# Kernel optimization log

Measured on AMD Instinct MI355X. Metric: run time of the kernel, lower is better.

## Reference

```python
import jax, jax.numpy as jnp
import numpy as np
import math

NUM_HEADS = 16


def _alibi_slopes(n):
    # n is a power of 2 here (16)
    start = 2.0 ** (-2.0 ** (-(math.log2(n) - 3)))
    return jnp.asarray([start * (start ** i) for i in range(n)], dtype=jnp.float32)


def setup_inputs() -> dict:
    key = jax.random.key(0)
    ks = jax.random.split(key, 7)
    B, S, D = 2, 2048, 1024
    s = 0.02
    return {
        "query": jax.random.normal(ks[0], (B, S, D), jnp.float32),
        "key": jax.random.normal(ks[1], (B, S, D), jnp.float32),
        "value": jax.random.normal(ks[2], (B, S, D), jnp.float32),
        "Wq": jax.random.normal(ks[3], (D, D), jnp.float32) * s,
        "Wk": jax.random.normal(ks[4], (D, D), jnp.float32) * s,
        "Wv": jax.random.normal(ks[5], (D, D), jnp.float32) * s,
        "Wo": jax.random.normal(ks[6], (D, D), jnp.float32) * s,
    }


def reference(query, key, value, Wq, Wk, Wv, Wo):
    B, S, D = query.shape
    H = NUM_HEADS
    hd = D // H
    scale = math.sqrt(hd)

    # projections (bias-free linears), split into heads: [B, S, H, hd]
    Q = (query @ Wq).reshape(B, S, H, hd)
    K = (key @ Wk).reshape(B, -1, H, hd)
    V = (value @ Wv).reshape(B, -1, H, hd)

    # attention scores [B, H, S, S]
    scores = jnp.einsum("bqhd,bkhd->bhqk", Q, K) / scale

    # ALiBi bias: -slope_h * |i - j|, broadcast over batch
    pos = jnp.arange(S, dtype=jnp.float32)
    rel = jnp.abs(pos[None, :] - pos[:, None])  # [S, S]
    slopes = _alibi_slopes(H)
    scores = scores - slopes[None, :, None, None] * rel[None, None, :, :]

    attn = jax.nn.softmax(scores, axis=-1)
    out = jnp.einsum("bhqk,bkhd->bqhd", attn, V).reshape(B, S, D)
    return out @ Wo
```

## Files before the change

### kernel.cpp

```cpp
#include <hip/hip_runtime.h>
#include <cstdint>
#include <cstddef>


typedef unsigned short u16;
typedef __attribute__((ext_vector_type(8))) _Float16 half8;
typedef __attribute__((ext_vector_type(4))) float f32x4;

#define DEVI static __device__ __forceinline__
#define MFMA16(a, b, c) __builtin_amdgcn_mfma_f32_16x16x32_f16(a, b, c, 0, 0, 0)

DEVI u16 f2h_bits(float f) {
  _Float16 h = (_Float16)f;
  union { _Float16 h; u16 u; } v; v.h = h;
  return v.u;
}

DEVI void gl_lds16(const u16* g, u16* l) {
  __builtin_amdgcn_global_load_lds(
      (const __attribute__((address_space(1))) void*)g,
      (__attribute__((address_space(3))) void*)l, 16, 0, 0);
}

__global__ __launch_bounds__(256) void cast3_h(const float* __restrict__ in0,
                                               const float* __restrict__ in1,
                                               const float* __restrict__ in2,
                                               u16* __restrict__ o0,
                                               u16* __restrict__ o1,
                                               u16* __restrict__ o2, int n) {
  const float* in = blockIdx.z == 0 ? in0 : (blockIdx.z == 1 ? in1 : in2);
  u16* out = blockIdx.z == 0 ? o0 : (blockIdx.z == 1 ? o1 : o2);
  int i = (blockIdx.x * 256 + threadIdx.x) * 4;
  if (i + 3 < n) {
    const float4 v = *(const float4*)(in + i);
    ushort4 o;
    o.x = f2h_bits(v.x); o.y = f2h_bits(v.y); o.z = f2h_bits(v.z); o.w = f2h_bits(v.w);
    *(ushort4*)(out + i) = o;
  }
}

__global__ __launch_bounds__(256) void transpose4_h(
    const float* __restrict__ W0, const float* __restrict__ W1,
    const float* __restrict__ W2, const float* __restrict__ W3,
    u16* __restrict__ T0, u16* __restrict__ T1, u16* __restrict__ T2,
    u16* __restrict__ T3) {
  const float* W = blockIdx.z == 0 ? W0 : (blockIdx.z == 1 ? W1 : (blockIdx.z == 2 ? W2 : W3));
  u16* Wt = blockIdx.z == 0 ? T0 : (blockIdx.z == 1 ? T1 : (blockIdx.z == 2 ? T2 : T3));
  __shared__ float tile[32][33];
  const int bx = blockIdx.x * 32;
  const int by = blockIdx.y * 32;
  const int x = threadIdx.x & 31;
  const int y0 = threadIdx.x >> 5;
#pragma unroll
  for (int i = y0; i < 32; i += 8)
    tile[i][x] = W[(size_t)(by + i) * 1024 + bx + x];
  __syncthreads();
#pragma unroll
  for (int i = y0; i < 32; i += 8)
    Wt[(size_t)(bx + i) * 1024 + by + x] = f2h_bits(tile[x][i]);
}

DEVI void gemm_body(const u16* __restrict__ A, const u16* __restrict__ Bt,
                    void* __restrict__ Cout, int mode, u16* As, u16* Bs) {
  constexpr int K = 1024, N = 1024;
  const int t = threadIdx.x;
  const int lane = t & 63;
  const int quad = lane >> 4;
  const int l16 = lane & 15;
  const int wid = t >> 6;
  const int mBase = blockIdx.y * 128;
  const int nBase = blockIdx.x * 128;
  const int wM = (wid >> 1) * 64;
  const int wN = (wid & 1) * 64;
  const int aswz = (quad ^ ((l16 >> 1) & 3)) << 3;

  f32x4 acc[4][4];
#pragma unroll
  for (int i = 0; i < 4; ++i)
#pragma unroll
    for (int j = 0; j < 4; ++j) acc[i][j] = (f32x4){0.f, 0.f, 0.f, 0.f};

  for (int kt = 0; kt < K / 32; ++kt) {
    const int kB = kt * 32;
    __syncthreads();
#pragma unroll
    for (int i = 0; i < 2; ++i) {
      const int ci = i * 256 + t;
      const int row = ci >> 2;
      const int col = (((ci & 3) ^ ((ci >> 3) & 3)) << 3);
      gl_lds16(A + (size_t)(mBase + row) * K + kB + col, As + ci * 8);
      gl_lds16(Bt + (size_t)(nBase + row) * K + kB + col, Bs + ci * 8);
    }
    __syncthreads();

    half8 a[4], b[4];
#pragma unroll
    for (int mi = 0; mi < 4; ++mi)
      a[mi] = *(const half8*)(As + (wM + mi * 16 + l16) * 32 + aswz);
#pragma unroll
    for (int ni = 0; ni < 4; ++ni)
      b[ni] = *(const half8*)(Bs + (wN + ni * 16 + l16) * 32 + aswz);
#pragma unroll
    for (int mi = 0; mi < 4; ++mi)
#pragma unroll
      for (int ni = 0; ni < 4; ++ni)
        acc[mi][ni] = MFMA16(a[mi], b[ni], acc[mi][ni]);
  }

#pragma unroll
  for (int mi = 0; mi < 4; ++mi) {
#pragma unroll
    for (int ni = 0; ni < 4; ++ni) {
#pragma unroll
      for (int r = 0; r < 4; ++r) {
        const int m = mBase + wM + mi * 16 + quad * 4 + r;
        const int n = nBase + wN + ni * 16 + l16;
        const float v = acc[mi][ni][r];
        if (mode == 0) {
          ((float*)Cout)[(size_t)m * N + n] = v;
        } else if (mode == 1) {
          ((u16*)Cout)[(size_t)m * N + n] = f2h_bits(v);
        } else {
          ((u16*)Cout)[(((size_t)(m >> 11) * 1024 + n) << 11) | (size_t)(m & 2047)] = f2h_bits(v);
        }
      }
    }
  }
}

__global__ __launch_bounds__(256) void proj_qkv(
    const u16* __restrict__ qb, const u16* __restrict__ kb, const u16* __restrict__ vb,
    const u16* __restrict__ Wqt, const u16* __restrict__ Wkt, const u16* __restrict__ Wvt,
    u16* __restrict__ Qp, u16* __restrict__ Kp, u16* __restrict__ Vtp) {
  __shared__ u16 As[128 * 32];
  __shared__ u16 Bs[128 * 32];
  const int z = blockIdx.z;
  const u16* A = z == 0 ? qb : (z == 1 ? kb : vb);
  const u16* Bt = z == 0 ? Wqt : (z == 1 ? Wkt : Wvt);
  void* C = z == 0 ? (void*)Qp : (z == 1 ? (void*)Kp : (void*)Vtp);
  gemm_body(A, Bt, C, z == 2 ? 2 : 1, As, Bs);
}

__global__ __launch_bounds__(256) void gemm_out(const u16* __restrict__ Ao,
                                                const u16* __restrict__ Wot,
                                                float* __restrict__ out) {
  __shared__ u16 As[128 * 32];
  __shared__ u16 Bs[128 * 32];
  gemm_body(Ao, Wot, out, 0, As, Bs);
}

__global__ __launch_bounds__(128, 2) void flash_alibi(
    const u16* __restrict__ Qg, const u16* __restrict__ Kg,
    const u16* __restrict__ Vtg, u16* __restrict__ Og) {
  constexpr int S = 2048, Dm = 1024, HD = 64;
  __shared__ u16 Qs[64 * 64];
  __shared__ u16 Ks[64 * 64];
  __shared__ u16 Vs[64 * 64];
  __shared__ u16 Ps[64 * 64];
  const int t = threadIdx.x, lane = t & 63, wid = t >> 6;
  const int quad = lane >> 4, l16 = lane & 15;
  const int qt = blockIdx.x, h = blockIdx.y, b = blockIdx.z;
  const int qBase = qt * 64;
  const size_t qRow0 = (size_t)b * S + qBase;
  const float sl2 = __builtin_amdgcn_exp2f(-0.5f * (float)(h + 1)) * 1.44269504f;
  const float sc2 = 0.125f * 1.44269504f;
  const int Di = (int)(30.0f / sl2);
  const int ktLo = max(0, (qBase - Di) >> 6);
  const int ktHi = min(31, (qBase + 63 + Di) >> 6);
  const int cswz = ((l16 & 7) << 3);

#pragma unroll
  for (int i = 0; i < 4; ++i) {
    const int ci = i * 128 + t;
    const int row = ci >> 3, col = (((ci & 7) ^ (row & 7)) << 3);
    gl_lds16(Qg + (qRow0 + row) * Dm + h * HD + col, Qs + ci * 8);
  }

  float bi[2][4];
#pragma unroll
  for (int m = 0; m < 2; ++m)
#pragma unroll
    for (int r = 0; r < 4; ++r)
      bi[m][r] = sl2 * (float)(qBase + wid * 32 + m * 16 + quad * 4 + r);

  f32x4 acc_o[2][4];
#pragma unroll
  for (int m = 0; m < 2; ++m)
#pragma unroll
    for (int nd = 0; nd < 4; ++nd) acc_o[m][nd] = (f32x4){0.f, 0.f, 0.f, 0.f};
  float lrow[2][4] = {{0.f, 0.f, 0.f, 0.f}, {0.f, 0.f, 0.f, 0.f}};

  const int pRowBase = wid * 32;

  for (int kt = ktLo; kt <= ktHi; ++kt) {
    const int kB = kt * 64;
    __syncthreads();
#pragma unroll
    for (int i = 0; i < 4; ++i) {
      const int ci = i * 128 + t;
      const int row = ci >> 3, col = (((ci & 7) ^ (row & 7)) << 3);
      gl_lds16(Kg + ((size_t)b * S + kB + row) * Dm + h * HD + col, Ks + ci * 8);
      gl_lds16(Vtg + ((size_t)(b * 16 + h) * HD + row) * S + kB + col, Vs + ci * 8);
    }
    __syncthreads();

    f32x4 s[2][4];
#pragma unroll
    for (int m = 0; m < 2; ++m)
#pragma unroll
      for (int ni = 0; ni < 4; ++ni) s[m][ni] = (f32x4){0.f, 0.f, 0.f, 0.f};
#pragma unroll
    for (int ks = 0; ks < 2; ++ks) {
      const int ck = ((ks * 4 + quad) << 3) ^ cswz;
      const half8 a0 = *(const half8*)(Qs + (wid * 32 + l16) * HD + ck);
      const half8 a1 = *(const half8*)(Qs + (wid * 32 + 16 + l16) * HD + ck);
#pragma unroll
      for (int ni = 0; ni < 4; ++ni) {
        const half8 bk = *(const half8*)(Ks + (ni * 16 + l16) * HD + ck);
        s[0][ni] = MFMA16(a0, bk, s[0][ni]);
        s[1][ni] = MFMA16(a1, bk, s[1][ni]);
      }
    }

    float bj[4];
#pragma unroll
    for (int ni = 0; ni < 4; ++ni) bj[ni] = sl2 * (float)(kB + ni * 16 + l16);
#pragma unroll
    for (int m = 0; m < 2; ++m) {
#pragma unroll
      for (int r = 0; r < 4; ++r) {
        float rs = 0.f;
        const int prow = (pRowBase + m * 16 + quad * 4 + r) * 64;
#pragma unroll
        for (int ni = 0; ni < 4; ++ni) {
          const float d = fabsf(bi[m][r] - bj[ni]);
          const float p = __builtin_amdgcn_exp2f(s[m][ni][r] * sc2 - d);
          rs += p;
          Ps[prow + ((ni * 16 + l16) ^ (quad << 4))] = f2h_bits(p);
        }
        lrow[m][r] += rs;
      }
    }
    __asm__ volatile("s_waitcnt lgkmcnt(0)" ::: "memory");

#pragma unroll
    for (int ks = 0; ks < 2; ++ks) {
      const int pk = (ks * 32 + quad * 8) ^ ((l16 & 12) << 2);
      const int ck = ((ks * 4 + quad) << 3) ^ cswz;
      const half8 aP0 = *(const half8*)(Ps + (pRowBase + l16) * 64 + pk);
      const half8 aP1 = *(const half8*)(Ps + (pRowBase + 16 + l16) * 64 + pk);
#pragma unroll
      for (int nd = 0; nd < 4; ++nd) {
        const half8 bv = *(const half8*)(Vs + (nd * 16 + l16) * HD + ck);
        acc_o[0][nd] = MFMA16(aP0, bv, acc_o[0][nd]);
        acc_o[1][nd] = MFMA16(aP1, bv, acc_o[1][nd]);
      }
    }
  }

#pragma unroll
  for (int m = 0; m < 2; ++m) {
#pragma unroll
    for (int r = 0; r < 4; ++r) {
      float l = lrow[m][r];
      l += __shfl_xor(l, 1);
      l += __shfl_xor(l, 2);
      l += __shfl_xor(l, 4);
      l += __shfl_xor(l, 8);
      const float inv = 1.f / l;
      const int rloc = wid * 32 + m * 16 + quad * 4 + r;
#pragma unroll
      for (int nd = 0; nd < 4; ++nd)
        Og[(qRow0 + rloc) * Dm + h * HD + nd * 16 + l16] = f2h_bits(acc_o[m][nd][r] * inv);
    }
  }
}

extern "C" void kernel_launch(void* const* d_in, const int* in_sizes, int n_in,
                              void* d_out, int out_size, void* d_ws, size_t ws_size,
                              hipStream_t stream) {
  const float* q  = (const float*)d_in[0];
  const float* k  = (const float*)d_in[1];
  const float* v  = (const float*)d_in[2];
  const float* Wq = (const float*)d_in[3];
  const float* Wk = (const float*)d_in[4];
  const float* Wv = (const float*)d_in[5];
  const float* Wo = (const float*)d_in[6];
  char* ws = (char*)d_ws;
  const size_t MB = 1ull << 20;
  u16* qb  = (u16*)(ws + 0 * MB);
  u16* kb  = (u16*)(ws + 8 * MB);
  u16* vb  = (u16*)(ws + 16 * MB);
  u16* Wqt = (u16*)(ws + 24 * MB);
  u16* Wkt = (u16*)(ws + 26 * MB);
  u16* Wvt = (u16*)(ws + 28 * MB);
  u16* Wot = (u16*)(ws + 30 * MB);
  u16* Qp  = (u16*)(ws + 32 * MB);
  u16* Kp  = (u16*)(ws + 40 * MB);
  u16* Vtp = (u16*)(ws + 48 * MB);
  u16* Ao  = (u16*)(ws + 56 * MB);

  const int n = 2 * 2048 * 1024;
  cast3_h<<<dim3(n / 1024, 1, 3), 256, 0, stream>>>(q, k, v, qb, kb, vb, n);
  transpose4_h<<<dim3(32, 32, 4), 256, 0, stream>>>(Wq, Wk, Wv, Wo, Wqt, Wkt, Wvt, Wot);
  proj_qkv<<<dim3(8, 32, 3), 256, 0, stream>>>(qb, kb, vb, Wqt, Wkt, Wvt, Qp, Kp, Vtp);
  flash_alibi<<<dim3(32, 16, 2), 128, 0, stream>>>(Qp, Kp, Vtp, Ao);
  gemm_out<<<dim3(8, 32), 256, 0, stream>>>(Ao, Wot, (float*)d_out);
}
```

Before: 244.3 us.

## Double-buffer K/V tiles in ALiBi flash kernel with four waves per block

The attention kernel now uses 256 threads with each wave handling 16 query rows instead of 32. K and V tiles are double-buffered in LDS so the next tile's global-to-LDS load is issued before computing the current one, leaving one barrier per iteration. Head order is reversed so the heads with the widest key windows are scheduled first, and s_setprio raises priority around the MFMA sections. This aims to hide load latency and improve occupancy and load balance, at the cost of more LDS and less register reuse of K/V fragments per wave.

```diff
diff --git a/kernel.cpp b/kernel.cpp
--- a/kernel.cpp
+++ b/kernel.cpp
@@ -149,17 +149,18 @@
   gemm_body(Ao, Wot, out, 0, As, Bs);
 }
 
-__global__ __launch_bounds__(128, 2) void flash_alibi(
+__global__ __launch_bounds__(256, 3) void flash_alibi(
     const u16* __restrict__ Qg, const u16* __restrict__ Kg,
     const u16* __restrict__ Vtg, u16* __restrict__ Og) {
   constexpr int S = 2048, Dm = 1024, HD = 64;
   __shared__ u16 Qs[64 * 64];
-  __shared__ u16 Ks[64 * 64];
-  __shared__ u16 Vs[64 * 64];
+  __shared__ u16 Ks[2][64 * 64];
+  __shared__ u16 Vs[2][64 * 64];
   __shared__ u16 Ps[64 * 64];
   const int t = threadIdx.x, lane = t & 63, wid = t >> 6;
   const int quad = lane >> 4, l16 = lane & 15;
-  const int qt = blockIdx.x, h = blockIdx.y, b = blockIdx.z;
+  const int qt = blockIdx.x, b = blockIdx.z;
+  const int h = 15 - blockIdx.y;
   const int qBase = qt * 64;
   const size_t qRow0 = (size_t)b * S + qBase;
   const float sl2 = __builtin_amdgcn_exp2f(-0.5f * (float)(h + 1)) * 1.44269504f;
@@ -168,111 +169,118 @@
   const int ktLo = max(0, (qBase - Di) >> 6);
   const int ktHi = min(31, (qBase + 63 + Di) >> 6);
   const int cswz = ((l16 & 7) << 3);
-
-#pragma unroll
-  for (int i = 0; i < 4; ++i) {
-    const int ci = i * 128 + t;
+  const int pRowBase = wid * 16;
+
+#pragma unroll
+  for (int i = 0; i < 2; ++i) {
+    const int ci = i * 256 + t;
     const int row = ci >> 3, col = (((ci & 7) ^ (row & 7)) << 3);
     gl_lds16(Qg + (qRow0 + row) * Dm + h * HD + col, Qs + ci * 8);
   }
-
-  float bi[2][4];
-#pragma unroll
-  for (int m = 0; m < 2; ++m)
-#pragma unroll
-    for (int r = 0; r < 4; ++r)
-      bi[m][r] = sl2 * (float)(qBase + wid * 32 + m * 16 + quad * 4 + r);
-
-  f32x4 acc_o[2][4];
-#pragma unroll
-  for (int m = 0; m < 2; ++m)
-#pragma unroll
-    for (int nd = 0; nd < 4; ++nd) acc_o[m][nd] = (f32x4){0.f, 0.f, 0.f, 0.f};
-  float lrow[2][4] = {{0.f, 0.f, 0.f, 0.f}, {0.f, 0.f, 0.f, 0.f}};
-
-  const int pRowBase = wid * 32;
+  {
+    const int kB = ktLo * 64;
+#pragma unroll
+    for (int i = 0; i < 2; ++i) {
+      const int ci = i * 256 + t;
+      const int row = ci >> 3, col = (((ci & 7) ^ (row & 7)) << 3);
+      gl_lds16(Kg + ((size_t)b * S + kB + row) * Dm + h * HD + col, Ks[0] + ci * 8);
+      gl_lds16(Vtg + ((size_t)(b * 16 + h) * HD + row) * S + kB + col, Vs[0] + ci * 8);
+    }
+  }
+
+  float bi[4];
+#pragma unroll
+  for (int r = 0; r < 4; ++r)
+    bi[r] = sl2 * (float)(qBase + wid * 16 + quad * 4 + r);
+
+  f32x4 acc_o[4];
+#pragma unroll
+  for (int nd = 0; nd < 4; ++nd) acc_o[nd] = (f32x4){0.f, 0.f, 0.f, 0.f};
+  float lrow[4] = {0.f, 0.f, 0.f, 0.f};
+
+  __syncthreads();
+  int bb = 0;
 
   for (int kt = ktLo; kt <= ktHi; ++kt) {
     const int kB = kt * 64;
-    __syncthreads();
-#pragma unroll
-    for (int i = 0; i < 4; ++i) {
-      const int ci = i * 128 + t;
-      const int row = ci >> 3, col = (((ci & 7) ^ (row & 7)) << 3);
-      gl_lds16(Kg + ((size_t)b * S + kB + row) * Dm + h * HD + col, Ks + ci * 8);
-      gl_lds16(Vtg + ((size_t)(b * 16 + h) * HD + row) * S + kB + col, Vs + ci * 8);
-    }
-    __syncthreads();
-
-    f32x4 s[2][4];
-#pragma unroll
-    for (int m = 0; m < 2; ++m)
-#pragma unroll
-      for (int ni = 0; ni < 4; ++ni) s[m][ni] = (f32x4){0.f, 0.f, 0.f, 0.f};
+    if (kt < ktHi) {
+      const int kBn = kB + 64;
+#pragma unroll
+      for (int i = 0; i < 2; ++i) {
+        const int ci = i * 256 + t;
+        const int row = ci >> 3, col = (((ci & 7) ^ (row & 7)) << 3);
+        gl_lds16(Kg + ((size_t)b * S + kBn + row) * Dm + h * HD + col, Ks[bb ^ 1] + ci * 8);
+        gl_lds16(Vtg + ((size_t)(b * 16 + h) * HD + row) * S + kBn + col, Vs[bb ^ 1] + ci * 8);
+      }
+    }
+
+    const u16* Kb = Ks[bb];
+    const u16* Vb = Vs[bb];
+
+    f32x4 s4[4];
+#pragma unroll
+    for (int ni = 0; ni < 4; ++ni) s4[ni] = (f32x4){0.f, 0.f, 0.f, 0.f};
+    __builtin_amdgcn_s_setprio(1);
 #pragma unroll
     for (int ks = 0; ks < 2; ++ks) {
       const int ck = ((ks * 4 + quad) << 3) ^ cswz;
-      const half8 a0 = *(const half8*)(Qs + (wid * 32 + l16) * HD + ck);
-      const half8 a1 = *(const half8*)(Qs + (wid * 32 + 16 + l16) * HD + ck);
+      const half8 a0 = *(const half8*)(Qs + (wid * 16 + l16) * HD + ck);
 #pragma unroll
       for (int ni = 0; ni < 4; ++ni) {
-        const half8 bk = *(const half8*)(Ks + (ni * 16 + l16) * HD + ck);
-        s[0][ni] = MFMA16(a0, bk, s[0][ni]);
-        s[1][ni] = MFMA16(a1, bk, s[1][ni]);
-      }
-    }
+        const half8 bk = *(const half8*)(Kb + (ni * 16 + l16) * HD + ck);
+        s4[ni] = MFMA16(a0, bk, s4[ni]);
+      }
+    }
+    __builtin_amdgcn_s_setprio(0);
 
     float bj[4];
 #pragma unroll
     for (int ni = 0; ni < 4; ++ni) bj[ni] = sl2 * (float)(kB + ni * 16 + l16);
 #pragma unroll
-    for (int m = 0; m < 2; ++m) {
-#pragma unroll
-      for (int r = 0; r < 4; ++r) {
-        float rs = 0.f;
-        const int prow = (pRowBase + m * 16 + quad * 4 + r) * 64;
-#pragma unroll
-        for (int ni = 0; ni < 4; ++ni) {
-          const float d = fabsf(bi[m][r] - bj[ni]);
-          const float p = __builtin_amdgcn_exp2f(s[m][ni][r] * sc2 - d);
-          rs += p;
-          Ps[prow + ((ni * 16 + l16) ^ (quad << 4))] = f2h_bits(p);
-        }
-        lrow[m][r] += rs;
-      }
+    for (int r = 0; r < 4; ++r) {
+      float rs = 0.f;
+      const int prow = (pRowBase + quad * 4 + r) * 64;
+#pragma unroll
+      for (int ni = 0; ni < 4; ++ni) {
+        const float d = fabsf(bi[r] - bj[ni]);
+        const float p = __builtin_amdgcn_exp2f(s4[ni][r] * sc2 - d);
+        rs += p;
+        Ps[prow + ((ni * 16 + l16) ^ (quad << 4))] = f2h_bits(p);
+      }
+      lrow[r] += rs;
     }
     __asm__ volatile("s_waitcnt lgkmcnt(0)" ::: "memory");
 
+    __builtin_amdgcn_s_setprio(1);
 #pragma unroll
     for (int ks = 0; ks < 2; ++ks) {
       const int pk = (ks * 32 + quad * 8) ^ ((l16 & 12) << 2);
       const int ck = ((ks * 4 + quad) << 3) ^ cswz;
-      const half8 aP0 = *(const half8*)(Ps + (pRowBase + l16) * 64 + pk);
-      const half8 aP1 = *(const half8*)(Ps + (pRowBase + 16 + l16) * 64 + pk);
+      const half8 aP = *(const half8*)(Ps + (pRowBase + l16) * 64 + pk);
 #pragma unroll
       for (int nd = 0; nd < 4; ++nd) {
-        const half8 bv = *(const half8*)(Vs + (nd * 16 + l16) * HD + ck);
-        acc_o[0][nd] = MFMA16(aP0, bv, acc_o[0][nd]);
-        acc_o[1][nd] = MFMA16(aP1, bv, acc_o[1][nd]);
-      }
-    }
-  }
-
-#pragma unroll
-  for (int m = 0; m < 2; ++m) {
-#pragma unroll
-    for (int r = 0; r < 4; ++r) {
-      float l = lrow[m][r];
-      l += __shfl_xor(l, 1);
-      l += __shfl_xor(l, 2);
-      l += __shfl_xor(l, 4);
-      l += __shfl_xor(l, 8);
-      const float inv = 1.f / l;
-      const int rloc = wid * 32 + m * 16 + quad * 4 + r;
-#pragma unroll
-      for (int nd = 0; nd < 4; ++nd)
-        Og[(qRow0 + rloc) * Dm + h * HD + nd * 16 + l16] = f2h_bits(acc_o[m][nd][r] * inv);
-    }
+        const half8 bv = *(const half8*)(Vb + (nd * 16 + l16) * HD + ck);
+        acc_o[nd] = MFMA16(aP, bv, acc_o[nd]);
+      }
+    }
+    __builtin_amdgcn_s_setprio(0);
+
+    __syncthreads();
+    bb ^= 1;
+  }
+
+#pragma unroll
+  for (int r = 0; r < 4; ++r) {
+    float l = lrow[r];
+    l += __shfl_xor(l, 1);
+    l += __shfl_xor(l, 2);
+    l += __shfl_xor(l, 4);
+    l += __shfl_xor(l, 8);
+    const float inv = 1.f / l;
+    const int rloc = wid * 16 + quad * 4 + r;
+#pragma unroll
+    for (int nd = 0; nd < 4; ++nd)
+      Og[(qRow0 + rloc) * Dm + h * HD + nd * 16 + l16] = f2h_bits(acc_o[nd][r] * inv);
   }
 }
 
@@ -304,6 +312,6 @@
   cast3_h<<<dim3(n / 1024, 1, 3), 256, 0, stream>>>(q, k, v, qb, kb, vb, n);
   transpose4_h<<<dim3(32, 32, 4), 256, 0, stream>>>(Wq, Wk, Wv, Wo, Wqt, Wkt, Wvt, Wot);
   proj_qkv<<<dim3(8, 32, 3), 256, 0, stream>>>(qb, kb, vb, Wqt, Wkt, Wvt, Qp, Kp, Vtp);
-  flash_alibi<<<dim3(32, 16, 2), 128, 0, stream>>>(Qp, Kp, Vtp, Ao);
+  flash_alibi<<<dim3(32, 16, 2), 256, 0, stream>>>(Qp, Kp, Vtp, Ao);
   gemm_out<<<dim3(8, 32), 256, 0, stream>>>(Ao, Wot, (float*)d_out);
 }
```

Result: faster. 228.7 us (-6.4%).
